# Performance work log

Measured on AMD Instinct MI355X. Metric: run time of the kernel, lower is better.

The kernel has to match this reference:

```python
import jax, jax.numpy as jnp
import numpy as np

N_ITEMS = 30000
N_USERS = 20000
N_NODES = N_ITEMS + N_USERS  # 50000
N_EDGES = 512000
D0, D1, D2 = 768, 128, 64
EPS = 1e-12  # torch F.normalize eps


def _xavier(key, shape):
    fan_in, fan_out = shape
    bound = np.sqrt(6.0 / (fan_in + fan_out)).astype(np.float32)
    return jax.random.uniform(key, shape, jnp.float32, -bound, bound)


def setup_inputs() -> dict:
    key = jax.random.key(0)
    ks = jax.random.split(key, 12)
    return {
        "item_embed": jax.random.normal(ks[0], (N_ITEMS, D0), jnp.float32) * 0.05,
        "user_embed": jax.random.normal(ks[1], (N_USERS, D0), jnp.float32) * 0.05,
        "W1_0": _xavier(ks[2], (D0, D1)),
        "b1_0": jnp.zeros((D1,), jnp.float32),
        "W2_0": _xavier(ks[3], (D0, D1)),
        "b2_0": jnp.zeros((D1,), jnp.float32),
        "W1_1": _xavier(ks[4], (D1, D2)),
        "b1_1": jnp.zeros((D2,), jnp.float32),
        "W2_1": _xavier(ks[5], (D1, D2)),
        "b2_1": jnp.zeros((D2,), jnp.float32),
        # normalized-Laplacian-like positive edge weights
        "edge_vals": jax.random.uniform(ks[6], (N_EDGES,), jnp.float32) * 0.1,
        "edge_rows": jax.random.randint(ks[7], (N_EDGES,), 0, N_NODES, jnp.int32),
        "edge_cols": jax.random.randint(ks[8], (N_EDGES,), 0, N_NODES, jnp.int32),
    }


def _ngcf_layer(ego, edge_vals, edge_rows, edge_cols, W1, b1, W2, b2):
    # side = A_in @ ego : gather source features, scale, segment-sum into rows
    msg = edge_vals[:, None] * ego[edge_cols]            # (E, d) gather
    side = jax.ops.segment_sum(msg, edge_rows, num_segments=N_NODES)
    side_plus_I = side + ego                             # (A + I) @ ego
    simple = side_plus_I @ W1 + b1                       # linear1
    interaction = (side * ego) @ W2 + b2                 # linear2 on Hadamard
    return jax.nn.leaky_relu(simple + interaction)       # dropout = eval/no-op


def reference(item_embed, user_embed, W1_0, b1_0, W2_0, b2_0,
              W1_1, b1_1, W2_1, b2_1, edge_vals, edge_rows, edge_cols):
    ego = jnp.concatenate([item_embed, user_embed], axis=0)  # (N, 768)
    all_embed = [ego]
    for (W1, b1, W2, b2) in ((W1_0, b1_0, W2_0, b2_0), (W1_1, b1_1, W2_1, b2_1)):
        ego = _ngcf_layer(ego, edge_vals, edge_rows, edge_cols, W1, b1, W2, b2)
        norm = jnp.maximum(jnp.linalg.norm(ego, axis=1, keepdims=True), EPS)
        all_embed.append(ego / norm)
    return jnp.concatenate(all_embed, axis=1)  # (N, 768+128+64)
```

## Files before the change

### kernel.cpp

```cpp
#include <hip/hip_runtime.h>
#include <stdint.h>

#define N_ITEMS 30000
#define N_USERS 20000
#define N_NODES 50000
#define N_EDGES 512000
#define D0 768
#define D1 128
#define D2 64
#define OSTRIDE 960

typedef short bf16x8 __attribute__((ext_vector_type(8)));
typedef float f32x4  __attribute__((ext_vector_type(4)));
typedef unsigned short u16x8 __attribute__((ext_vector_type(8)));
typedef unsigned short u16x4 __attribute__((ext_vector_type(4)));
typedef unsigned short u16x2 __attribute__((ext_vector_type(2)));

__device__ __forceinline__ unsigned short f2bf(float x) {
    union { float f; uint32_t u; } v; v.f = x;
    uint32_t u = v.u;
    return (unsigned short)((u + 0x7FFF + ((u >> 16) & 1)) >> 16);
}
__device__ __forceinline__ float bf2f(unsigned short s) {
    union { uint32_t u; float f; } v; v.u = ((uint32_t)s) << 16; return v.f;
}

__global__ __launch_bounds__(256) void copy_ego0(const float* __restrict__ item,
                                                 const float* __restrict__ user,
                                                 float* __restrict__ out,
                                                 unsigned short* __restrict__ outb) {
    int idx = blockIdx.x * 256 + threadIdx.x;
    if (idx >= N_NODES * (D0 / 4)) return;
    int row = idx / (D0 / 4);
    int c4  = idx % (D0 / 4);
    const float4* src = (row < N_ITEMS)
        ? (const float4*)(item + (size_t)row * D0)
        : (const float4*)(user + (size_t)(row - N_ITEMS) * D0);
    float4 v = src[c4];
    *(float4*)(out + (size_t)row * OSTRIDE + c4 * 4) = v;
    if (outb) {
        u16x4 b;
        b[0] = f2bf(v.x); b[1] = f2bf(v.y); b[2] = f2bf(v.z); b[3] = f2bf(v.w);
        *(u16x4*)(outb + (size_t)row * D0 + c4 * 4) = b;
    }
}

__global__ __launch_bounds__(256) void histogram_kernel(const int* __restrict__ rows,
                                                        int* __restrict__ counts) {
    int e = blockIdx.x * 256 + threadIdx.x;
    if (e < N_EDGES) atomicAdd(&counts[rows[e]], 1);
}

#define SCAN_THREADS 1024
__global__ __launch_bounds__(1024) void scan_kernel(const int* __restrict__ counts,
                                                    int* __restrict__ offsets,
                                                    int* __restrict__ cursors) {
    __shared__ int partials[SCAN_THREADS];
    const int CH = (N_NODES + SCAN_THREADS - 1) / SCAN_THREADS;
    int t = threadIdx.x;
    int base = t * CH;
    int sum = 0;
    for (int i = 0; i < CH; i++) {
        int idx = base + i;
        if (idx < N_NODES) sum += counts[idx];
    }
    partials[t] = sum;
    __syncthreads();
    for (int off = 1; off < SCAN_THREADS; off <<= 1) {
        int add = (t >= off) ? partials[t - off] : 0;
        __syncthreads();
        partials[t] += add;
        __syncthreads();
    }
    int run = (t == 0) ? 0 : partials[t - 1];
    for (int i = 0; i < CH; i++) {
        int idx = base + i;
        if (idx < N_NODES) {
            offsets[idx] = run;
            cursors[idx] = run;
            run += counts[idx];
        }
    }
    if (t == SCAN_THREADS - 1) offsets[N_NODES] = N_EDGES;
}

__global__ __launch_bounds__(256) void fill_kernel(const float* __restrict__ vals,
                                                   const int* __restrict__ rows,
                                                   const int* __restrict__ cols,
                                                   int* __restrict__ cursors,
                                                   float* __restrict__ svals,
                                                   int* __restrict__ scols) {
    int e = blockIdx.x * 256 + threadIdx.x;
    if (e >= N_EDGES) return;
    int pos = atomicAdd(&cursors[rows[e]], 1);
    svals[pos] = vals[e];
    scols[pos] = cols[e];
}

template <int K, int N>
__global__ __launch_bounds__(256) void prep_wb(const float* __restrict__ W,
                                               unsigned short* __restrict__ Wb) {
    constexpr int FR = (K / 32) * (N / 16);
    int tid = blockIdx.x * 256 + threadIdx.x;
    if (tid >= FR * 64) return;
    int frag = tid >> 6, lane = tid & 63;
    int kk = frag / (N / 16), nt = frag % (N / 16);
    int quad = lane >> 4, n = lane & 15;
    unsigned short tmp[8];
#pragma unroll
    for (int jj = 0; jj < 8; jj++) {
        int k = kk * 32 + quad * 8 + jj;
        tmp[jj] = f2bf(W[(size_t)k * N + nt * 16 + n]);
    }
#pragma unroll
    for (int jj = 0; jj < 8; jj++) Wb[(size_t)tid * 8 + jj] = tmp[jj];
}

template <int DIN, int DOUT, int THREADS, bool BSRC>
__global__ __launch_bounds__(THREADS, (THREADS == 512 ? 6 : 4)) void fused_layer_mfma(
    const int*   __restrict__ offsets,
    const float* __restrict__ svals,
    const int*   __restrict__ scols,
    const float* __restrict__ ego, int ego_stride,
    const unsigned short* __restrict__ egob,
    const unsigned short* __restrict__ Wb1,
    const unsigned short* __restrict__ Wb2,
    const float* __restrict__ b1, const float* __restrict__ b2,
    float* __restrict__ out, int out_stride,
    unsigned short* __restrict__ outb)
{
    constexpr int NPB   = 16;
    constexpr int WAVES = THREADS / 64;
    constexpr int NPW   = NPB / WAVES;
    constexpr int KK    = DIN / 32;
    constexpr int NT    = DOUT / 16;
    constexpr int NTW   = NT / WAVES;
    constexpr int PAD   = 8;

    __shared__ unsigned short s_sum [NPB][DIN + PAD];
    __shared__ unsigned short s_prod[NPB][DIN + PAD];

    const int t = threadIdx.x;
    const int w = t >> 6, l = t & 63;
    const int node_base = blockIdx.x * NPB;

    for (int nn = 0; nn < NPW; nn++) {
        int n   = w * NPW + nn;
        int row = node_base + n;
        int beg = offsets[row], end = offsets[row + 1];

        if constexpr (BSRC && DIN == 768) {
            u16x8 eg0 = *(const u16x8*)(egob + (size_t)row * 768 + l * 8);
            u16x4 eg1 = *(const u16x4*)(egob + (size_t)row * 768 + 512 + l * 4);
            float acc0[8] = {0.f, 0.f, 0.f, 0.f, 0.f, 0.f, 0.f, 0.f};
            float acc1[4] = {0.f, 0.f, 0.f, 0.f};

            for (int base = beg; base < end; base += 64) {
                int cnt = min(64, end - base);
                int   cl = 0;
                float vl = 0.f;
                if (l < cnt) { cl = scols[base + l]; vl = svals[base + l]; }
                int u = 0;
                for (; u + 4 <= cnt; u += 4) {
                    const unsigned short* sp0 = egob + (size_t)__shfl(cl, u + 0) * 768;
                    const unsigned short* sp1 = egob + (size_t)__shfl(cl, u + 1) * 768;
                    const unsigned short* sp2 = egob + (size_t)__shfl(cl, u + 2) * 768;
                    const unsigned short* sp3 = egob + (size_t)__shfl(cl, u + 3) * 768;
                    float v0 = __shfl(vl, u + 0), v1 = __shfl(vl, u + 1);
                    float v2 = __shfl(vl, u + 2), v3 = __shfl(vl, u + 3);
                    u16x8 a0 = *(const u16x8*)(sp0 + l * 8);
                    u16x8 a1 = *(const u16x8*)(sp1 + l * 8);
                    u16x8 a2 = *(const u16x8*)(sp2 + l * 8);
                    u16x8 a3 = *(const u16x8*)(sp3 + l * 8);
                    u16x4 c0 = *(const u16x4*)(sp0 + 512 + l * 4);
                    u16x4 c1 = *(const u16x4*)(sp1 + 512 + l * 4);
                    u16x4 c2 = *(const u16x4*)(sp2 + 512 + l * 4);
                    u16x4 c3 = *(const u16x4*)(sp3 + 512 + l * 4);
#pragma unroll
                    for (int j = 0; j < 8; j++) {
                        acc0[j] = fmaf(v0, bf2f(a0[j]), acc0[j]);
                        acc0[j] = fmaf(v1, bf2f(a1[j]), acc0[j]);
                        acc0[j] = fmaf(v2, bf2f(a2[j]), acc0[j]);
                        acc0[j] = fmaf(v3, bf2f(a3[j]), acc0[j]);
                    }
#pragma unroll
                    for (int j = 0; j < 4; j++) {
                        acc1[j] = fmaf(v0, bf2f(c0[j]), acc1[j]);
                        acc1[j] = fmaf(v1, bf2f(c1[j]), acc1[j]);
                        acc1[j] = fmaf(v2, bf2f(c2[j]), acc1[j]);
                        acc1[j] = fmaf(v3, bf2f(c3[j]), acc1[j]);
                    }
                }
                for (; u < cnt; u++) {
                    const unsigned short* sp = egob + (size_t)__shfl(cl, u) * 768;
                    float v0 = __shfl(vl, u);
                    u16x8 a0 = *(const u16x8*)(sp + l * 8);
                    u16x4 c0 = *(const u16x4*)(sp + 512 + l * 4);
#pragma unroll
                    for (int j = 0; j < 8; j++) acc0[j] = fmaf(v0, bf2f(a0[j]), acc0[j]);
#pragma unroll
                    for (int j = 0; j < 4; j++) acc1[j] = fmaf(v0, bf2f(c0[j]), acc1[j]);
                }
            }
            u16x8 s0, p0; u16x4 s1, p1;
#pragma unroll
            for (int j = 0; j < 8; j++) {
                float e = bf2f(eg0[j]);
                s0[j] = f2bf(acc0[j] + e);
                p0[j] = f2bf(acc0[j] * e);
            }
#pragma unroll
            for (int j = 0; j < 4; j++) {
                float e = bf2f(eg1[j]);
                s1[j] = f2bf(acc1[j] + e);
                p1[j] = f2bf(acc1[j] * e);
            }
            *(u16x8*)&s_sum [n][l * 8] = s0;
            *(u16x8*)&s_prod[n][l * 8] = p0;
            *(u16x4*)&s_sum [n][512 + l * 4] = s1;
            *(u16x4*)&s_prod[n][512 + l * 4] = p1;
        } else if constexpr (BSRC && DIN == 128) {
            u16x2 eg = *(const u16x2*)(egob + (size_t)row * 128 + l * 2);
            float acc[2] = {0.f, 0.f};
            for (int base = beg; base < end; base += 64) {
                int cnt = min(64, end - base);
                int   cl = 0;
                float vl = 0.f;
                if (l < cnt) { cl = scols[base + l]; vl = svals[base + l]; }
                int u = 0;
                for (; u + 4 <= cnt; u += 4) {
                    const unsigned short* sp0 = egob + (size_t)__shfl(cl, u + 0) * 128;
                    const unsigned short* sp1 = egob + (size_t)__shfl(cl, u + 1) * 128;
                    const unsigned short* sp2 = egob + (size_t)__shfl(cl, u + 2) * 128;
                    const unsigned short* sp3 = egob + (size_t)__shfl(cl, u + 3) * 128;
                    float v0 = __shfl(vl, u + 0), v1 = __shfl(vl, u + 1);
                    float v2 = __shfl(vl, u + 2), v3 = __shfl(vl, u + 3);
                    u16x2 a0 = *(const u16x2*)(sp0 + l * 2);
                    u16x2 a1 = *(const u16x2*)(sp1 + l * 2);
                    u16x2 a2 = *(const u16x2*)(sp2 + l * 2);
                    u16x2 a3 = *(const u16x2*)(sp3 + l * 2);
#pragma unroll
                    for (int j = 0; j < 2; j++) {
                        acc[j] = fmaf(v0, bf2f(a0[j]), acc[j]);
                        acc[j] = fmaf(v1, bf2f(a1[j]), acc[j]);
                        acc[j] = fmaf(v2, bf2f(a2[j]), acc[j]);
                        acc[j] = fmaf(v3, bf2f(a3[j]), acc[j]);
                    }
                }
                for (; u < cnt; u++) {
                    const unsigned short* sp = egob + (size_t)__shfl(cl, u) * 128;
                    float v0 = __shfl(vl, u);
                    u16x2 a0 = *(const u16x2*)(sp + l * 2);
                    acc[0] = fmaf(v0, bf2f(a0[0]), acc[0]);
                    acc[1] = fmaf(v0, bf2f(a0[1]), acc[1]);
                }
            }
            u16x2 s, p;
            float e0 = bf2f(eg[0]), e1 = bf2f(eg[1]);
            s[0] = f2bf(acc[0] + e0); p[0] = f2bf(acc[0] * e0);
            s[1] = f2bf(acc[1] + e1); p[1] = f2bf(acc[1] * e1);
            *(u16x2*)&s_sum [n][l * 2] = s;
            *(u16x2*)&s_prod[n][l * 2] = p;
        } else {
            constexpr int CW = (DIN >= 256) ? 4 : 2;
            constexpr int NC = DIN / (64 * CW);
            float acc[NC * CW], eg[NC * CW];
#pragma unroll
            for (int c = 0; c < NC * CW; c++) acc[c] = 0.f;
#pragma unroll
            for (int c = 0; c < NC; c++) {
#pragma unroll
                for (int j = 0; j < CW; j++)
                    eg[c * CW + j] = ego[(size_t)row * ego_stride + c * 64 * CW + l * CW + j];
            }
            for (int base = beg; base < end; base += 64) {
                int cnt = min(64, end - base);
                int   cl = 0;
                float vl = 0.f;
                if (l < cnt) { cl = scols[base + l]; vl = svals[base + l]; }
                for (int u = 0; u < cnt; u++) {
                    const float* sp = ego + (size_t)__shfl(cl, u) * ego_stride;
                    float v0 = __shfl(vl, u);
#pragma unroll
                    for (int c = 0; c < NC; c++) {
#pragma unroll
                        for (int j = 0; j < CW; j++)
                            acc[c * CW + j] = fmaf(v0, sp[c * 64 * CW + l * CW + j], acc[c * CW + j]);
                    }
                }
            }
#pragma unroll
            for (int c = 0; c < NC * CW; c++) {
                int col = (c / CW) * 64 * CW + l * CW + (c % CW);
                s_sum [n][col] = f2bf(acc[c] + eg[c]);
                s_prod[n][col] = f2bf(acc[c] * eg[c]);
            }
        }
    }
    __syncthreads();

    const int m = l & 15, quad = l >> 4;
    f32x4 accc[NTW] = {};
    for (int kk = 0; kk < KK; kk++) {
        bf16x8 a_s = *(const bf16x8*)&s_sum [m][kk * 32 + quad * 8];
        bf16x8 a_p = *(const bf16x8*)&s_prod[m][kk * 32 + quad * 8];
#pragma unroll
        for (int i = 0; i < NTW; i++) {
            int nt = w * NTW + i;
            bf16x8 bf1 = *(const bf16x8*)(Wb1 + ((size_t)(kk * NT + nt) * 64 + l) * 8);
            bf16x8 bf2 = *(const bf16x8*)(Wb2 + ((size_t)(kk * NT + nt) * 64 + l) * 8);
            accc[i] = __builtin_amdgcn_mfma_f32_16x16x32_bf16(a_s, bf1, accc[i], 0, 0, 0);
            accc[i] = __builtin_amdgcn_mfma_f32_16x16x32_bf16(a_p, bf2, accc[i], 0, 0, 0);
        }
    }

#pragma unroll
    for (int i = 0; i < NTW; i++) {
        int nt = w * NTW + i;
        int j  = nt * 16 + m;
        float bb = b1[j] + b2[j];
#pragma unroll
        for (int r = 0; r < 4; r++) {
            int node  = node_base + quad * 4 + r;
            float val = accc[i][r] + bb;
            val = val > 0.f ? val : 0.01f * val;
            out[(size_t)node * out_stride + j] = val;
            if (outb) outb[(size_t)node * DOUT + j] = f2bf(val);
        }
    }
}

__global__ __launch_bounds__(256) void normalize_kernel(float* __restrict__ out) {
    int row  = blockIdx.x * 4 + (threadIdx.x >> 6);
    int lane = threadIdx.x & 63;
    float* p1 = out + (size_t)row * OSTRIDE + D0;
    float* p2 = p1 + D1;

    float2 v = *(float2*)(p1 + lane * 2);
    float ss = v.x * v.x + v.y * v.y;
#pragma unroll
    for (int off = 32; off > 0; off >>= 1) ss += __shfl_xor(ss, off, 64);
    float inv1 = 1.0f / fmaxf(sqrtf(ss), 1e-12f);
    v.x *= inv1; v.y *= inv1;
    *(float2*)(p1 + lane * 2) = v;

    float wv = p2[lane];
    float ss2 = wv * wv;
#pragma unroll
    for (int off = 32; off > 0; off >>= 1) ss2 += __shfl_xor(ss2, off, 64);
    p2[lane] = wv / fmaxf(sqrtf(ss2), 1e-12f);
}

extern "C" void kernel_launch(void* const* d_in, const int* in_sizes, int n_in,
                              void* d_out, int out_size, void* d_ws, size_t ws_size,
                              hipStream_t stream) {
    const float* item  = (const float*)d_in[0];
    const float* user  = (const float*)d_in[1];
    const float* W1_0  = (const float*)d_in[2];
    const float* b1_0  = (const float*)d_in[3];
    const float* W2_0  = (const float*)d_in[4];
    const float* b2_0  = (const float*)d_in[5];
    const float* W1_1  = (const float*)d_in[6];
    const float* b1_1  = (const float*)d_in[7];
    const float* W2_1  = (const float*)d_in[8];
    const float* b2_1  = (const float*)d_in[9];
    const float* evals = (const float*)d_in[10];
    const int*   erows = (const int*)d_in[11];
    const int*   ecols = (const int*)d_in[12];
    float* out = (float*)d_out;

    int*   counts  = (int*)d_ws;
    int*   offsets = counts + N_NODES;
    int*   cursors = offsets + (N_NODES + 1);
    float* svals   = (float*)((int*)d_ws + 150004);
    int*   scols   = (int*)(svals + N_EDGES);
    unsigned short* wb1_0 = (unsigned short*)(scols + N_EDGES);
    unsigned short* wb2_0 = wb1_0 + (size_t)D0 * D1;
    unsigned short* wb1_1 = wb2_0 + (size_t)D0 * D1;
    unsigned short* wb2_1 = wb1_1 + (size_t)D1 * D2;
    unsigned short* ego0b = wb2_1 + (size_t)D1 * D2;
    unsigned short* ego1b = ego0b + (size_t)N_NODES * D0;

    const size_t need = 5122000 + (size_t)N_NODES * D0 * 2 + (size_t)N_NODES * D1 * 2;
    const bool big = ws_size >= need;

    copy_ego0<<<(N_NODES * (D0 / 4) + 255) / 256, 256, 0, stream>>>(
        item, user, out, big ? ego0b : nullptr);

    hipMemsetAsync(counts, 0, (size_t)N_NODES * sizeof(int), stream);
    histogram_kernel<<<(N_EDGES + 255) / 256, 256, 0, stream>>>(erows, counts);
    scan_kernel<<<1, SCAN_THREADS, 0, stream>>>(counts, offsets, cursors);
    fill_kernel<<<(N_EDGES + 255) / 256, 256, 0, stream>>>(evals, erows, ecols,
                                                           cursors, svals, scols);

    {
        constexpr int FR0 = (D0 / 32) * (D1 / 16);
        constexpr int FR1 = (D1 / 32) * (D2 / 16);
        prep_wb<D0, D1><<<(FR0 * 64 + 255) / 256, 256, 0, stream>>>(W1_0, wb1_0);
        prep_wb<D0, D1><<<(FR0 * 64 + 255) / 256, 256, 0, stream>>>(W2_0, wb2_0);
        prep_wb<D1, D2><<<(FR1 * 64 + 255) / 256, 256, 0, stream>>>(W1_1, wb1_1);
        prep_wb<D1, D2><<<(FR1 * 64 + 255) / 256, 256, 0, stream>>>(W2_1, wb2_1);
    }

    if (big) {
        fused_layer_mfma<D0, D1, 512, true><<<N_NODES / 16, 512, 0, stream>>>(
            offsets, svals, scols, out, OSTRIDE, ego0b,
            wb1_0, wb2_0, b1_0, b2_0, out + D0, OSTRIDE, ego1b);
        fused_layer_mfma<D1, D2, 256, true><<<N_NODES / 16, 256, 0, stream>>>(
            offsets, svals, scols, out + D0, OSTRIDE, ego1b,
            wb1_1, wb2_1, b1_1, b2_1, out + D0 + D1, OSTRIDE, nullptr);
    } else {
        fused_layer_mfma<D0, D1, 512, false><<<N_NODES / 16, 512, 0, stream>>>(
            offsets, svals, scols, out, OSTRIDE, nullptr,
            wb1_0, wb2_0, b1_0, b2_0, out + D0, OSTRIDE, nullptr);
        fused_layer_mfma<D1, D2, 256, false><<<N_NODES / 16, 256, 0, stream>>>(
            offsets, svals, scols, out + D0, OSTRIDE, nullptr,
            wb1_1, wb2_1, b1_1, b2_1, out + D0 + D1, OSTRIDE, nullptr);
    }

    normalize_kernel<<<N_NODES / 4, 256, 0, stream>>>(out);
}
```

Measured before the change: 705.4 us.

## Fuse memset, histogram, weight prep and normalization into neighboring kernels

Zeroing of the row-count array moves into the ego copy kernel. The edge histogram and the four bf16 weight-fragment prep launches are merged into one aux kernel that splits work by block index. The separate L2-normalize pass is removed: the layer-2 kernel stages its output in shared memory, normalizes it, and also normalizes the layer-1 fp32 slice in place. This cuts several launches and one extra pass over the output, but layer 2 now rewrites layer-1 fp32 rows that other blocks may still read in the non-bf16 fallback path.

Result: faster. 686.3 us (-2.7%).

```diff
diff --git a/kernel.cpp b/kernel.cpp
--- a/kernel.cpp
+++ b/kernel.cpp
@@ -28,8 +28,10 @@
 __global__ __launch_bounds__(256) void copy_ego0(const float* __restrict__ item,
                                                  const float* __restrict__ user,
                                                  float* __restrict__ out,
-                                                 unsigned short* __restrict__ outb) {
+                                                 unsigned short* __restrict__ outb,
+                                                 int* __restrict__ counts) {
     int idx = blockIdx.x * 256 + threadIdx.x;
+    if (idx < N_NODES) counts[idx] = 0;
     if (idx >= N_NODES * (D0 / 4)) return;
     int row = idx / (D0 / 4);
     int c4  = idx % (D0 / 4);
@@ -45,10 +47,43 @@
     }
 }
 
-__global__ __launch_bounds__(256) void histogram_kernel(const int* __restrict__ rows,
-                                                        int* __restrict__ counts) {
-    int e = blockIdx.x * 256 + threadIdx.x;
-    if (e < N_EDGES) atomicAdd(&counts[rows[e]], 1);
+template <int K, int N>
+__device__ __forceinline__ void prep_body(const float* __restrict__ W,
+                                          unsigned short* __restrict__ Wb, int tid) {
+    constexpr int FR = (K / 32) * (N / 16);
+    if (tid >= FR * 64) return;
+    int frag = tid >> 6, lane = tid & 63;
+    int kk = frag / (N / 16), nt = frag % (N / 16);
+    int quad = lane >> 4, n = lane & 15;
+    unsigned short tmp[8];
+#pragma unroll
+    for (int jj = 0; jj < 8; jj++) {
+        int k = kk * 32 + quad * 8 + jj;
+        tmp[jj] = f2bf(W[(size_t)k * N + nt * 16 + n]);
+    }
+#pragma unroll
+    for (int jj = 0; jj < 8; jj++) Wb[(size_t)tid * 8 + jj] = tmp[jj];
+}
+
+__global__ __launch_bounds__(256) void aux_kernel(
+    const int* __restrict__ erows, int* __restrict__ counts,
+    const float* __restrict__ W1_0, const float* __restrict__ W2_0,
+    const float* __restrict__ W1_1, const float* __restrict__ W2_1,
+    unsigned short* __restrict__ wb1_0, unsigned short* __restrict__ wb2_0,
+    unsigned short* __restrict__ wb1_1, unsigned short* __restrict__ wb2_1) {
+    int b = blockIdx.x, t = threadIdx.x;
+    if (b < 2000) {
+        int e = b * 256 + t;
+        atomicAdd(&counts[erows[e]], 1);
+    } else if (b < 2048) {
+        prep_body<D0, D1>(W1_0, wb1_0, (b - 2000) * 256 + t);
+    } else if (b < 2096) {
+        prep_body<D0, D1>(W2_0, wb2_0, (b - 2048) * 256 + t);
+    } else if (b < 2100) {
+        prep_body<D1, D2>(W1_1, wb1_1, (b - 2096) * 256 + t);
+    } else {
+        prep_body<D1, D2>(W2_1, wb2_1, (b - 2100) * 256 + t);
+    }
 }
 
 #define SCAN_THREADS 1024
@@ -97,26 +132,7 @@
     scols[pos] = cols[e];
 }
 
-template <int K, int N>
-__global__ __launch_bounds__(256) void prep_wb(const float* __restrict__ W,
-                                               unsigned short* __restrict__ Wb) {
-    constexpr int FR = (K / 32) * (N / 16);
-    int tid = blockIdx.x * 256 + threadIdx.x;
-    if (tid >= FR * 64) return;
-    int frag = tid >> 6, lane = tid & 63;
-    int kk = frag / (N / 16), nt = frag % (N / 16);
-    int quad = lane >> 4, n = lane & 15;
-    unsigned short tmp[8];
-#pragma unroll
-    for (int jj = 0; jj < 8; jj++) {
-        int k = kk * 32 + quad * 8 + jj;
-        tmp[jj] = f2bf(W[(size_t)k * N + nt * 16 + n]);
-    }
-#pragma unroll
-    for (int jj = 0; jj < 8; jj++) Wb[(size_t)tid * 8 + jj] = tmp[jj];
-}
-
-template <int DIN, int DOUT, int THREADS, bool BSRC>
+template <int DIN, int DOUT, int THREADS, bool BSRC, bool FUSE_NORM>
 __global__ __launch_bounds__(THREADS, (THREADS == 512 ? 6 : 4)) void fused_layer_mfma(
     const int*   __restrict__ offsets,
     const float* __restrict__ svals,
@@ -127,7 +143,8 @@
     const unsigned short* __restrict__ Wb2,
     const float* __restrict__ b1, const float* __restrict__ b2,
     float* __restrict__ out, int out_stride,
-    unsigned short* __restrict__ outb)
+    unsigned short* __restrict__ outb,
+    float* __restrict__ ego1_f32)
 {
     constexpr int NPB   = 16;
     constexpr int WAVES = THREADS / 64;
@@ -139,6 +156,7 @@
 
     __shared__ unsigned short s_sum [NPB][DIN + PAD];
     __shared__ unsigned short s_prod[NPB][DIN + PAD];
+    __shared__ float s_o2[FUSE_NORM ? NPB : 1][FUSE_NORM ? (DOUT + 4) : 1];
 
     const int t = threadIdx.x;
     const int w = t >> 6, l = t & 63;
@@ -324,31 +342,37 @@
             int node  = node_base + quad * 4 + r;
             float val = accc[i][r] + bb;
             val = val > 0.f ? val : 0.01f * val;
-            out[(size_t)node * out_stride + j] = val;
-            if (outb) outb[(size_t)node * DOUT + j] = f2bf(val);
+            if constexpr (FUSE_NORM) {
+                s_o2[quad * 4 + r][j] = val;
+            } else {
+                out[(size_t)node * out_stride + j] = val;
+                if (outb) outb[(size_t)node * DOUT + j] = f2bf(val);
+            }
         }
     }
-}
-
-__global__ __launch_bounds__(256) void normalize_kernel(float* __restrict__ out) {
-    int row  = blockIdx.x * 4 + (threadIdx.x >> 6);
-    int lane = threadIdx.x & 63;
-    float* p1 = out + (size_t)row * OSTRIDE + D0;
-    float* p2 = p1 + D1;
-
-    float2 v = *(float2*)(p1 + lane * 2);
-    float ss = v.x * v.x + v.y * v.y;
-#pragma unroll
-    for (int off = 32; off > 0; off >>= 1) ss += __shfl_xor(ss, off, 64);
-    float inv1 = 1.0f / fmaxf(sqrtf(ss), 1e-12f);
-    v.x *= inv1; v.y *= inv1;
-    *(float2*)(p1 + lane * 2) = v;
-
-    float wv = p2[lane];
-    float ss2 = wv * wv;
-#pragma unroll
-    for (int off = 32; off > 0; off >>= 1) ss2 += __shfl_xor(ss2, off, 64);
-    p2[lane] = wv / fmaxf(sqrtf(ss2), 1e-12f);
+
+    if constexpr (FUSE_NORM) {
+        __syncthreads();
+        static_assert(!FUSE_NORM || (DOUT == 64 && WAVES == 4), "fuse-norm layout");
+#pragma unroll
+        for (int nn = 0; nn < 4; nn++) {
+            int nl  = w * 4 + nn;
+            int row = node_base + nl;
+            float v2 = s_o2[nl][l];
+            float ss2 = v2 * v2;
+#pragma unroll
+            for (int off = 32; off > 0; off >>= 1) ss2 += __shfl_xor(ss2, off, 64);
+            out[(size_t)row * out_stride + l] = v2 / fmaxf(sqrtf(ss2), 1e-12f);
+            float* p1 = ego1_f32 + (size_t)row * out_stride;
+            float2 v1 = *(float2*)(p1 + l * 2);
+            float ss1 = v1.x * v1.x + v1.y * v1.y;
+#pragma unroll
+            for (int off = 32; off > 0; off >>= 1) ss1 += __shfl_xor(ss1, off, 64);
+            float inv1 = 1.0f / fmaxf(sqrtf(ss1), 1e-12f);
+            v1.x *= inv1; v1.y *= inv1;
+            *(float2*)(p1 + l * 2) = v1;
+        }
+    }
 }
 
 extern "C" void kernel_launch(void* const* d_in, const int* in_sizes, int n_in,
@@ -385,38 +409,27 @@
     const bool big = ws_size >= need;
 
     copy_ego0<<<(N_NODES * (D0 / 4) + 255) / 256, 256, 0, stream>>>(
-        item, user, out, big ? ego0b : nullptr);
-
-    hipMemsetAsync(counts, 0, (size_t)N_NODES * sizeof(int), stream);
-    histogram_kernel<<<(N_EDGES + 255) / 256, 256, 0, stream>>>(erows, counts);
+        item, user, out, big ? ego0b : nullptr, counts);
+
+    aux_kernel<<<2104, 256, 0, stream>>>(erows, counts, W1_0, W2_0, W1_1, W2_1,
+                                         wb1_0, wb2_0, wb1_1, wb2_1);
     scan_kernel<<<1, SCAN_THREADS, 0, stream>>>(counts, offsets, cursors);
     fill_kernel<<<(N_EDGES + 255) / 256, 256, 0, stream>>>(evals, erows, ecols,
                                                            cursors, svals, scols);
 
-    {
-        constexpr int FR0 = (D0 / 32) * (D1 / 16);
-        constexpr int FR1 = (D1 / 32) * (D2 / 16);
-        prep_wb<D0, D1><<<(FR0 * 64 + 255) / 256, 256, 0, stream>>>(W1_0, wb1_0);
-        prep_wb<D0, D1><<<(FR0 * 64 + 255) / 256, 256, 0, stream>>>(W2_0, wb2_0);
-        prep_wb<D1, D2><<<(FR1 * 64 + 255) / 256, 256, 0, stream>>>(W1_1, wb1_1);
-        prep_wb<D1, D2><<<(FR1 * 64 + 255) / 256, 256, 0, stream>>>(W2_1, wb2_1);
-    }
-
     if (big) {
-        fused_layer_mfma<D0, D1, 512, true><<<N_NODES / 16, 512, 0, stream>>>(
+        fused_layer_mfma<D0, D1, 512, true, false><<<N_NODES / 16, 512, 0, stream>>>(
             offsets, svals, scols, out, OSTRIDE, ego0b,
-            wb1_0, wb2_0, b1_0, b2_0, out + D0, OSTRIDE, ego1b);
-        fused_layer_mfma<D1, D2, 256, true><<<N_NODES / 16, 256, 0, stream>>>(
+            wb1_0, wb2_0, b1_0, b2_0, out + D0, OSTRIDE, ego1b, nullptr);
+        fused_layer_mfma<D1, D2, 256, true, true><<<N_NODES / 16, 256, 0, stream>>>(
             offsets, svals, scols, out + D0, OSTRIDE, ego1b,
-            wb1_1, wb2_1, b1_1, b2_1, out + D0 + D1, OSTRIDE, nullptr);
+            wb1_1, wb2_1, b1_1, b2_1, out + D0 + D1, OSTRIDE, nullptr, out + D0);
     } else {
-        fused_layer_mfma<D0, D1, 512, false><<<N_NODES / 16, 512, 0, stream>>>(
+        fused_layer_mfma<D0, D1, 512, false, false><<<N_NODES / 16, 512, 0, stream>>>(
             offsets, svals, scols, out, OSTRIDE, nullptr,
-            wb1_0, wb2_0, b1_0, b2_0, out + D0, OSTRIDE, nullptr);
-        fused_layer_mfma<D1, D2, 256, false><<<N_NODES / 16, 256, 0, stream>>>(
+            wb1_0, wb2_0, b1_0, b2_0, out + D0, OSTRIDE, nullptr, nullptr);
+        fused_layer_mfma<D1, D2, 256, false, true><<<N_NODES / 16, 256, 0, stream>>>(
             offsets, svals, scols, out + D0, OSTRIDE, nullptr,
-            wb1_1, wb2_1, b1_1, b2_1, out + D0 + D1, OSTRIDE, nullptr);
-    }
-
-    normalize_kernel<<<N_NODES / 4, 256, 0, stream>>>(out);
-}
+            wb1_1, wb2_1, b1_1, b2_1, out + D0 + D1, OSTRIDE, nullptr, out + D0);
+    }
+}
```
